# Performance work log

Measured on AMD Instinct MI355X. Metric: run time of the kernel, lower is better.

## Reference

```python
import math
import jax, jax.numpy as jnp
import numpy as np

B, S, HID = 1, 2048, 2048
H, D = 32, 64            # heads, head_dim = HID // H
THETA = 10000.0
EPS = 1e-6
LAYER_IDX = 12
LAM_INIT = 0.8 - 0.6 * math.exp(-0.3 * LAYER_IDX)  # lambda_init_fn(layer_idx)
SCALE = 1.0 / math.sqrt(D)


def _rope_cos_sin(seq_len, dim):
    inv_freq = 1.0 / (THETA ** (np.arange(0, dim, 2, dtype=np.float64) / dim))
    freqs = np.outer(np.arange(seq_len, dtype=np.float64), inv_freq)
    emb = np.concatenate([freqs, freqs], axis=-1)  # [S, D] (llama duplicates freqs)
    return jnp.asarray(np.cos(emb), jnp.float32), jnp.asarray(np.sin(emb), jnp.float32)


def _rotate_half(x):
    return jnp.concatenate([-x[..., D // 2:], x[..., : D // 2]], axis=-1)


def _apply_rope(x, cos, sin):
    # x: [B, H, S, D]; cos/sin: [S, D] broadcast over B, H
    return x * cos + _rotate_half(x) * sin


def setup_inputs() -> dict:
    key = jax.random.key(0)
    ks = jax.random.split(key, 10)
    return {
        "hidden_states": jax.random.normal(ks[0], (B, S, HID), jnp.float32),
        "Wq": jax.random.normal(ks[1], (2 * HID, HID), jnp.float32) * 0.02,
        "Wk": jax.random.normal(ks[2], (2 * HID, HID), jnp.float32) * 0.02,
        "Wv": jax.random.normal(ks[3], (HID, HID), jnp.float32) * 0.02,
        "Wo": jax.random.normal(ks[4], (HID, HID), jnp.float32) * 0.02,
        "lambda_q1": jax.random.normal(ks[5], (D,), jnp.float32) * 0.1,
        "lambda_k1": jax.random.normal(ks[6], (D,), jnp.float32) * 0.1,
        "lambda_q2": jax.random.normal(ks[7], (D,), jnp.float32) * 0.1,
        "lambda_k2": jax.random.normal(ks[8], (D,), jnp.float32) * 0.1,
        "subln_w": jnp.ones((D,), jnp.float32),
    }


def reference(hidden_states, Wq, Wk, Wv, Wo,
              lambda_q1, lambda_k1, lambda_q2, lambda_k2, subln_w):
    # Projections (nn.Linear, no bias): x @ W.T
    q = hidden_states @ Wq.T                       # [B, S, 2*HID]
    k = hidden_states @ Wk.T                       # [B, S, 2*HID]
    v = hidden_states @ Wv.T                       # [B, S, HID]

    def to_heads(t):  # [B, S, H*D] -> [B, H, S, D]
        return t.reshape(B, S, H, D).transpose(0, 2, 1, 3)

    q1, q2 = jnp.split(q, 2, axis=-1)
    k1, k2 = jnp.split(k, 2, axis=-1)
    q1, q2, k1, k2, v = map(to_heads, (q1, q2, k1, k2, v))

    cos, sin = _rope_cos_sin(S, D)
    q1, k1 = _apply_rope(q1, cos, sin), _apply_rope(k1, cos, sin)
    q2, k2 = _apply_rope(q2, cos, sin), _apply_rope(k2, cos, sin)

    # Causal additive mask [S, S]
    causal = jnp.tril(jnp.ones((S, S), bool))
    neg_inf = jnp.finfo(jnp.float32).min
    mask = jnp.where(causal, 0.0, neg_inf)

    s1 = jnp.einsum("bhqd,bhkd->bhqk", q1, k1) * SCALE + mask
    s2 = jnp.einsum("bhqd,bhkd->bhqk", q2, k2) * SCALE + mask

    lam = (jnp.exp(jnp.sum(lambda_q1 * lambda_k1))
           - jnp.exp(jnp.sum(lambda_q2 * lambda_k2)) + LAM_INIT)

    attn_w = jax.nn.softmax(s1, axis=-1) - lam * jax.nn.softmax(s2, axis=-1)
    attn = jnp.einsum("bhqk,bhkd->bhqd", attn_w, v)  # [B, H, S, D]

    # Head-wise RMSNorm (LlamaRMSNorm over value_head_dim)
    var = jnp.mean(jnp.square(attn), axis=-1, keepdims=True)
    attn = attn * jax.lax.rsqrt(var + EPS) * subln_w
    attn = attn * (1.0 - LAM_INIT)

    out = attn.transpose(0, 2, 1, 3).reshape(B, S, HID) @ Wo.T
    return out
```

## Files before the change

kernel.cpp:

```cpp
#include <hip/hip_runtime.h>


typedef __bf16 bf16;
typedef __bf16 bf16x4 __attribute__((ext_vector_type(4)));
typedef __bf16 bf16x8 __attribute__((ext_vector_type(8)));
typedef float  f32x4  __attribute__((ext_vector_type(4)));

#define MFMA(a, b, c) __builtin_amdgcn_mfma_f32_16x16x32_bf16((a), (b), (c), 0, 0, 0)

#define S_LEN   2048
#define HID_DIM 2048
#define NHEAD   32
#define HD      64
#define QKV_N   10240
#define LAM_INIT 0.7836057665316245f
#define ONE_MINUS_LAM_INIT 0.21639423346837553f
#define QSCALE  0.18033688011112042f
#define RMS_EPS 1e-6f

__device__ __forceinline__ void gld16(const void* g, void* l) {
    __builtin_amdgcn_global_load_lds(
        (const __attribute__((address_space(1))) void*)g,
        (__attribute__((address_space(3))) void*)l, 16, 0, 0);
}

__global__ void cvt_f32_bf16(const float* __restrict__ src, bf16* __restrict__ dst, int n) {
    int i = (blockIdx.x * 256 + threadIdx.x) * 4;
    if (i + 3 < n) {
        float4 v = *(const float4*)(src + i);
        bf16x4 o = { (bf16)v.x, (bf16)v.y, (bf16)v.z, (bf16)v.w };
        *(bf16x4*)(dst + i) = o;
    }
}

__global__ void lam_kernel(const float* __restrict__ lq1, const float* __restrict__ lk1,
                           const float* __restrict__ lq2, const float* __restrict__ lk2,
                           float* __restrict__ out) {
    int t = threadIdx.x;
    float a = lq1[t] * lk1[t];
    float b = lq2[t] * lk2[t];
    #pragma unroll
    for (int off = 32; off > 0; off >>= 1) {
        a += __shfl_xor(a, off, 64);
        b += __shfl_xor(b, off, 64);
    }
    if (t == 0) out[0] = expf(a) - expf(b) + LAM_INIT;
}

template<int OUT_BF16>
__global__ __launch_bounds__(256, 2)
void gemm_bt(const bf16* __restrict__ A, const bf16* __restrict__ B,
             void* __restrict__ Cout, int M, int N, int K) {
    __shared__ __align__(16) bf16 As[128 * 32];
    __shared__ __align__(16) bf16 Bs[128 * 32];
    const int tid  = threadIdx.x;
    const int wave = tid >> 6, lane = tid & 63;
    const int wm = wave >> 1, wn = wave & 1;
    const int l = lane & 15, quad = lane >> 4;
    const int m0 = blockIdx.y * 128, n0 = blockIdx.x * 128;

    f32x4 acc[4][4];
    #pragma unroll
    for (int i = 0; i < 4; ++i)
        #pragma unroll
        for (int j = 0; j < 4; ++j) acc[i][j] = (f32x4){0.f, 0.f, 0.f, 0.f};

    const int r0 = tid >> 2, c0 = (tid & 3) * 8;
    const bf16* Ag = A + (size_t)(m0 + r0) * K + c0;
    const bf16* Bg = B + (size_t)(n0 + r0) * K + c0;
    bf16* As0 = As + tid * 8;
    bf16* Bs0 = Bs + tid * 8;

    for (int kt = 0; kt < K; kt += 32) {
        __syncthreads();
        gld16(Ag + kt, As0);
        gld16(Ag + (size_t)64 * K + kt, As0 + 2048);
        gld16(Bg + kt, Bs0);
        gld16(Bg + (size_t)64 * K + kt, Bs0 + 2048);
        __syncthreads();

        bf16x8 af[4], bfr[4];
        #pragma unroll
        for (int mi = 0; mi < 4; ++mi)
            af[mi] = *(const bf16x8*)(As + (wm * 64 + mi * 16 + l) * 32 + quad * 8);
        #pragma unroll
        for (int ni = 0; ni < 4; ++ni)
            bfr[ni] = *(const bf16x8*)(Bs + (wn * 64 + ni * 16 + l) * 32 + quad * 8);
        #pragma unroll
        for (int mi = 0; mi < 4; ++mi)
            #pragma unroll
            for (int ni = 0; ni < 4; ++ni)
                acc[mi][ni] = MFMA(af[mi], bfr[ni], acc[mi][ni]);
    }

    #pragma unroll
    for (int mi = 0; mi < 4; ++mi)
        #pragma unroll
        for (int ni = 0; ni < 4; ++ni)
            #pragma unroll
            for (int r = 0; r < 4; ++r) {
                const int row = m0 + wm * 64 + mi * 16 + quad * 4 + r;
                const int col = n0 + wn * 64 + ni * 16 + l;
                const float v = acc[mi][ni][r];
                if (OUT_BF16) ((bf16*)Cout)[(size_t)row * N + col] = (bf16)v;
                else          ((float*)Cout)[(size_t)row * N + col] = v;
            }
}

__global__ __launch_bounds__(256)
void rope_split(const bf16* __restrict__ qkv,
                bf16* __restrict__ Q1, bf16* __restrict__ K1,
                bf16* __restrict__ Q2, bf16* __restrict__ K2,
                bf16* __restrict__ Vt) {
    const int h = blockIdx.y;
    const int s0 = blockIdx.x * 64;
    const int t = threadIdx.x;
    const int d = t & 63, sr = t >> 6;
    __shared__ __align__(16) bf16 vt_lds[64][72];

    const int i = d & 31;
    const float invf = exp2f(-(float)i * 0.4152410118609203f);
    const float sign = (d < 32) ? -1.0f : 1.0f;

    for (int it = 0; it < 16; ++it) {
        const int s = s0 + it * 4 + sr;
        const bf16* row = qkv + (size_t)s * QKV_N;
        const int cb  = h * 64 + d;
        const int cbo = h * 64 + (d ^ 32);
        const float ang = (float)s * invf;
        const float cs = cosf(ang), sn = sinf(ang);
        const float q1v = (float)row[cb],         q1o = (float)row[cbo];
        const float q2v = (float)row[2048 + cb],  q2o = (float)row[2048 + cbo];
        const float k1v = (float)row[4096 + cb],  k1o = (float)row[4096 + cbo];
        const float k2v = (float)row[6144 + cb],  k2o = (float)row[6144 + cbo];
        const float vv  = (float)row[8192 + cb];
        const size_t o = ((size_t)h * S_LEN + s) * HD + d;
        Q1[o] = (bf16)((q1v * cs + sign * q1o * sn) * QSCALE);
        Q2[o] = (bf16)((q2v * cs + sign * q2o * sn) * QSCALE);
        K1[o] = (bf16)(k1v * cs + sign * k1o * sn);
        K2[o] = (bf16)(k2v * cs + sign * k2o * sn);
        vt_lds[d][it * 4 + sr] = (bf16)vv;
    }
    __syncthreads();
    const int dd = t >> 2, cg = t & 3;
    bf16x8 w0 = *(const bf16x8*)(&vt_lds[dd][cg * 16]);
    bf16x8 w1 = *(const bf16x8*)(&vt_lds[dd][cg * 16 + 8]);
    bf16* dst = Vt + ((size_t)h * HD + dd) * S_LEN + s0 + cg * 16;
    *(bf16x8*)(dst)     = w0;
    *(bf16x8*)(dst + 8) = w1;
}

__global__ __launch_bounds__(256, 2)
void diff_attn(const bf16* __restrict__ Q1, const bf16* __restrict__ K1,
               const bf16* __restrict__ Q2, const bf16* __restrict__ K2,
               const bf16* __restrict__ Vt, const float* __restrict__ lam_p,
               const float* __restrict__ subln_w, bf16* __restrict__ attn_out) {
    const int bid  = blockIdx.x;
    const int h    = (bid >> 1) & 31;
    const int idx  = bid >> 6;
    const int qb   = (bid & 1) ? idx : (15 - idx);
    const int q0   = qb * 128;
    const int tid  = threadIdx.x;
    const int wave = tid >> 6, lane = tid & 63;
    const int sid  = wave >> 1, half = wave & 1;
    const int l    = lane & 15, quad = lane >> 4;
    const int q0w  = q0 + half * 64;

    __shared__ __align__(16) char smem[61440];
    bf16* K1s = (bf16*)smem;
    bf16* K2s = (bf16*)(smem + 8192);
    bf16* Vts = (bf16*)(smem + 16384);
    bf16* Pw  = (bf16*)(smem + 24576 + wave * 9216);

    const bf16* Qh  = (sid ? Q2 : Q1) + ((size_t)h * S_LEN + q0w) * HD;
    const bf16* K1g = K1 + (size_t)h * S_LEN * HD;
    const bf16* K2g = K2 + (size_t)h * S_LEN * HD;
    const bf16* Vtg = Vt + (size_t)h * HD * S_LEN;
    const bf16* Ksm = sid ? K2s : K1s;

    const int rr  = tid >> 3;
    const int csw = ((tid & 7) ^ (rr & 7)) * 8;
    bf16* l1 = K1s + tid * 8;
    bf16* l2 = K2s + tid * 8;
    bf16* lv = Vts + tid * 8;

    bf16x8 qf[4][2];
    #pragma unroll
    for (int ni = 0; ni < 4; ++ni)
        #pragma unroll
        for (int ks = 0; ks < 2; ++ks)
            qf[ni][ks] = *(const bf16x8*)(Qh + (ni * 16 + l) * HD + ks * 32 + quad * 8);

    f32x4 O[4][4];
    #pragma unroll
    for (int mi = 0; mi < 4; ++mi)
        #pragma unroll
        for (int ni = 0; ni < 4; ++ni)
            O[mi][ni] = (f32x4){0.f, 0.f, 0.f, 0.f};
    float csum[4] = {0.f, 0.f, 0.f, 0.f};

    const int T = 2 * qb + 2;
    const int sw8 = l & 7;
    for (int t = 0; t < T; ++t) {
        const int kv0 = t * 64;
        __syncthreads();
        {
            const bf16* k1p = K1g + (size_t)(kv0 + rr) * HD + csw;
            const bf16* k2p = K2g + (size_t)(kv0 + rr) * HD + csw;
            const bf16* vtp = Vtg + (size_t)rr * S_LEN + kv0 + csw;
            gld16(k1p, l1);
            gld16(k1p + (size_t)32 * HD, l1 + 2048);
            gld16(k2p, l2);
            gld16(k2p + (size_t)32 * HD, l2 + 2048);
            gld16(vtp, lv);
            gld16(vtp + (size_t)32 * S_LEN, lv + 2048);
        }
        __syncthreads();

        if (kv0 <= q0w) {
            const bool diag = (kv0 == q0w);

            #pragma unroll
            for (int mi = 0; mi < 4; ++mi) {
                const int krow = (mi * 16 + l) * 64;
                bf16x8 ka0 = *(const bf16x8*)(Ksm + krow + ((quad ^ sw8) << 3));
                bf16x8 ka1 = *(const bf16x8*)(Ksm + krow + (((4 + quad) ^ sw8) << 3));
                #pragma unroll
                for (int ni = 0; ni < 4; ++ni) {
                    f32x4 c = (f32x4){0.f, 0.f, 0.f, 0.f};
                    c = MFMA(ka0, qf[ni][0], c);
                    c = MFMA(ka1, qf[ni][1], c);
                    bf16x4 pk;
                    float lsum = 0.f;
                    #pragma unroll
                    for (int r = 0; r < 4; ++r) {
                        float p = __builtin_amdgcn_exp2f(c[r]);
                        if (diag && (mi * 16 + quad * 4 + r > ni * 16 + l)) p = 0.f;
                        lsum += p;
                        pk[r] = (bf16)p;
                    }
                    csum[ni] += lsum;
                    *(bf16x4*)(Pw + (ni * 16 + l) * 72 + mi * 16 + quad * 4) = pk;
                }
            }

            bf16x8 vb[2][4];
            #pragma unroll
            for (int ks = 0; ks < 2; ++ks)
                #pragma unroll
                for (int ni = 0; ni < 4; ++ni)
                    vb[ks][ni] = *(const bf16x8*)(Vts + (ni * 16 + l) * 64 +
                                                  ((((ks << 2) + quad) ^ sw8) << 3));

            asm volatile("s_waitcnt lgkmcnt(0)" ::: "memory");

            #pragma unroll
            for (int ks = 0; ks < 2; ++ks) {
                bf16x8 pa[4];
                #pragma unroll
                for (int mi = 0; mi < 4; ++mi)
                    pa[mi] = *(const bf16x8*)(Pw + (mi * 16 + l) * 72 + ks * 32 + quad * 8);
                #pragma unroll
                for (int ni = 0; ni < 4; ++ni)
                    #pragma unroll
                    for (int mi = 0; mi < 4; ++mi)
                        O[mi][ni] = MFMA(pa[mi], vb[ks][ni], O[mi][ni]);
            }
        }
    }

    __syncthreads();
    float* epi = (float*)(smem + half * 16640);

    #pragma unroll
    for (int ni = 0; ni < 4; ++ni) {
        csum[ni] += __shfl_xor(csum[ni], 16, 64);
        csum[ni] += __shfl_xor(csum[ni], 32, 64);
    }

    if (sid == 1) {
        const float lam = lam_p[0];
        #pragma unroll
        for (int mi = 0; mi < 4; ++mi)
            #pragma unroll
            for (int r = 0; r < 4; ++r) {
                const float inv = lam / __shfl(csum[mi], quad * 4 + r, 64);
                const int row = mi * 16 + quad * 4 + r;
                #pragma unroll
                for (int ni = 0; ni < 4; ++ni)
                    epi[row * 65 + ni * 16 + l] = O[mi][ni][r] * inv;
            }
    }
    __syncthreads();

    if (sid == 0) {
        float sw[4];
        #pragma unroll
        for (int ni = 0; ni < 4; ++ni) sw[ni] = subln_w[ni * 16 + l];

        #pragma unroll
        for (int mi = 0; mi < 4; ++mi) {
            float inv1[4];
            #pragma unroll
            for (int r = 0; r < 4; ++r)
                inv1[r] = 1.0f / __shfl(csum[mi], quad * 4 + r, 64);

            float v[4][4]; float ssq[4] = {0.f, 0.f, 0.f, 0.f};
            #pragma unroll
            for (int ni = 0; ni < 4; ++ni)
                #pragma unroll
                for (int r = 0; r < 4; ++r) {
                    const int row = mi * 16 + quad * 4 + r;
                    const float x = O[mi][ni][r] * inv1[r] - epi[row * 65 + ni * 16 + l];
                    v[ni][r] = x;
                    ssq[r] += x * x;
                }
            #pragma unroll
            for (int r = 0; r < 4; ++r) {
                float s = ssq[r];
                s += __shfl_xor(s, 1, 64);
                s += __shfl_xor(s, 2, 64);
                s += __shfl_xor(s, 4, 64);
                s += __shfl_xor(s, 8, 64);
                ssq[r] = rsqrtf(s * (1.0f / 64.0f) + RMS_EPS) * ONE_MINUS_LAM_INIT;
            }
            #pragma unroll
            for (int ni = 0; ni < 4; ++ni)
                #pragma unroll
                for (int r = 0; r < 4; ++r) {
                    const int row = q0w + mi * 16 + quad * 4 + r;
                    attn_out[(size_t)row * HID_DIM + h * 64 + ni * 16 + l] =
                        (bf16)(v[ni][r] * ssq[r] * sw[ni]);
                }
        }
    }
}

extern "C" void kernel_launch(void* const* d_in, const int* in_sizes, int n_in,
                              void* d_out, int out_size, void* d_ws, size_t ws_size,
                              hipStream_t stream) {
    const float* hs  = (const float*)d_in[0];
    const float* Wq  = (const float*)d_in[1];
    const float* Wk  = (const float*)d_in[2];
    const float* Wv  = (const float*)d_in[3];
    const float* Wo  = (const float*)d_in[4];
    const float* lq1 = (const float*)d_in[5];
    const float* lk1 = (const float*)d_in[6];
    const float* lq2 = (const float*)d_in[7];
    const float* lk2 = (const float*)d_in[8];
    const float* slw = (const float*)d_in[9];

    if (ws_size < 151000000u) return;

    char* ws = (char*)d_ws;
    bf16*  hsb  = (bf16*)(ws);
    bf16*  Wb   = (bf16*)(ws + 8388608);
    bf16*  Wob  = (bf16*)(ws + 50331648);
    bf16*  qkv  = (bf16*)(ws + 58720256);
    bf16*  Q1b  = (bf16*)(ws + 100663296);
    bf16*  K1b  = (bf16*)(ws + 109051904);
    bf16*  Q2b  = (bf16*)(ws + 117440512);
    bf16*  K2b  = (bf16*)(ws + 125829120);
    bf16*  Vtb  = (bf16*)(ws + 134217728);
    bf16*  abuf = (bf16*)(ws + 142606336);
    float* lamp = (float*)(ws + 150994944);

    cvt_f32_bf16<<<4096, 256, 0, stream>>>(hs, hsb, 4194304);
    cvt_f32_bf16<<<8192, 256, 0, stream>>>(Wq, Wb, 8388608);
    cvt_f32_bf16<<<8192, 256, 0, stream>>>(Wk, Wb + 8388608, 8388608);
    cvt_f32_bf16<<<4096, 256, 0, stream>>>(Wv, Wb + 16777216, 4194304);
    cvt_f32_bf16<<<4096, 256, 0, stream>>>(Wo, Wob, 4194304);
    lam_kernel<<<1, 64, 0, stream>>>(lq1, lk1, lq2, lk2, lamp);

    gemm_bt<1><<<dim3(QKV_N / 128, S_LEN / 128), 256, 0, stream>>>(
        hsb, Wb, qkv, S_LEN, QKV_N, HID_DIM);

    rope_split<<<dim3(S_LEN / 64, NHEAD), 256, 0, stream>>>(qkv, Q1b, K1b, Q2b, K2b, Vtb);

    diff_attn<<<512, 256, 0, stream>>>(Q1b, K1b, Q2b, K2b, Vtb, lamp, slw, abuf);

    gemm_bt<0><<<dim3(HID_DIM / 128, S_LEN / 128), 256, 0, stream>>>(
        abuf, Wob, d_out, S_LEN, HID_DIM, HID_DIM);
}
```

Baseline: 405.1 us.

## Merge conversion kernels, widen GEMM K-tile with swizzled LDS, split-K output projection

New measurement: 369.4 us. -8.8%, faster.

```diff
diff --git a/kernel.cpp b/kernel.cpp
--- a/kernel.cpp
+++ b/kernel.cpp
@@ -24,40 +24,52 @@
         (__attribute__((address_space(3))) void*)l, 16, 0, 0);
 }
 
-__global__ void cvt_f32_bf16(const float* __restrict__ src, bf16* __restrict__ dst, int n) {
-    int i = (blockIdx.x * 256 + threadIdx.x) * 4;
-    if (i + 3 < n) {
-        float4 v = *(const float4*)(src + i);
-        bf16x4 o = { (bf16)v.x, (bf16)v.y, (bf16)v.z, (bf16)v.w };
-        *(bf16x4*)(dst + i) = o;
-    }
-}
-
-__global__ void lam_kernel(const float* __restrict__ lq1, const float* __restrict__ lk1,
-                           const float* __restrict__ lq2, const float* __restrict__ lk2,
-                           float* __restrict__ out) {
-    int t = threadIdx.x;
-    float a = lq1[t] * lk1[t];
-    float b = lq2[t] * lk2[t];
-    #pragma unroll
-    for (int off = 32; off > 0; off >>= 1) {
-        a += __shfl_xor(a, off, 64);
-        b += __shfl_xor(b, off, 64);
-    }
-    if (t == 0) out[0] = expf(a) - expf(b) + LAM_INIT;
-}
-
-template<int OUT_BF16>
-__global__ __launch_bounds__(256, 2)
+__global__ void cvt_all(const float* __restrict__ hs, const float* __restrict__ Wq,
+                        const float* __restrict__ Wk, const float* __restrict__ Wv,
+                        const float* __restrict__ Wo,
+                        const float* __restrict__ lq1, const float* __restrict__ lk1,
+                        const float* __restrict__ lq2, const float* __restrict__ lk2,
+                        bf16* __restrict__ hsb, bf16* __restrict__ Wb,
+                        bf16* __restrict__ Wob, float* __restrict__ lam_out) {
+    const int bid = blockIdx.x;
+    if (bid >= 28672) {
+        const int t = threadIdx.x;
+        if (t < 64) {
+            float a = lq1[t] * lk1[t];
+            float b = lq2[t] * lk2[t];
+            #pragma unroll
+            for (int off = 32; off > 0; off >>= 1) {
+                a += __shfl_xor(a, off, 64);
+                b += __shfl_xor(b, off, 64);
+            }
+            if (t == 0) lam_out[0] = expf(a) - expf(b) + LAM_INIT;
+        }
+        return;
+    }
+    const float* src; bf16* dst; int off;
+    if      (bid <  4096) { src = hs; dst = hsb;            off = bid;         }
+    else if (bid < 12288) { src = Wq; dst = Wb;             off = bid - 4096;  }
+    else if (bid < 20480) { src = Wk; dst = Wb +  8388608;  off = bid - 12288; }
+    else if (bid < 24576) { src = Wv; dst = Wb + 16777216;  off = bid - 20480; }
+    else                  { src = Wo; dst = Wob;            off = bid - 24576; }
+    const int i = off * 1024 + threadIdx.x * 4;
+    float4 v = *(const float4*)(src + i);
+    bf16x4 o = { (bf16)v.x, (bf16)v.y, (bf16)v.z, (bf16)v.w };
+    *(bf16x4*)(dst + i) = o;
+}
+
+template<int OUT_MODE>
+__global__ __launch_bounds__(256, 3)
 void gemm_bt(const bf16* __restrict__ A, const bf16* __restrict__ B,
-             void* __restrict__ Cout, int M, int N, int K) {
-    __shared__ __align__(16) bf16 As[128 * 32];
-    __shared__ __align__(16) bf16 Bs[128 * 32];
+             void* __restrict__ Cout, int M, int N, int K_total, int K_part) {
+    __shared__ __align__(16) bf16 As[128 * 64];
+    __shared__ __align__(16) bf16 Bs[128 * 64];
     const int tid  = threadIdx.x;
     const int wave = tid >> 6, lane = tid & 63;
     const int wm = wave >> 1, wn = wave & 1;
     const int l = lane & 15, quad = lane >> 4;
     const int m0 = blockIdx.y * 128, n0 = blockIdx.x * 128;
+    const int kz = blockIdx.z * K_part;
 
     f32x4 acc[4][4];
     #pragma unroll
@@ -65,34 +77,40 @@
         #pragma unroll
         for (int j = 0; j < 4; ++j) acc[i][j] = (f32x4){0.f, 0.f, 0.f, 0.f};
 
-    const int r0 = tid >> 2, c0 = (tid & 3) * 8;
-    const bf16* Ag = A + (size_t)(m0 + r0) * K + c0;
-    const bf16* Bg = B + (size_t)(n0 + r0) * K + c0;
-    bf16* As0 = As + tid * 8;
-    bf16* Bs0 = Bs + tid * 8;
-
-    for (int kt = 0; kt < K; kt += 32) {
+    const int rr  = tid >> 3;
+    const int csw = ((tid & 7) ^ (rr & 7)) * 8;
+    const bf16* Ag = A + (size_t)(m0 + rr) * K_total + kz + csw;
+    const bf16* Bg = B + (size_t)(n0 + rr) * K_total + kz + csw;
+
+    for (int kt = 0; kt < K_part; kt += 64) {
         __syncthreads();
-        gld16(Ag + kt, As0);
-        gld16(Ag + (size_t)64 * K + kt, As0 + 2048);
-        gld16(Bg + kt, Bs0);
-        gld16(Bg + (size_t)64 * K + kt, Bs0 + 2048);
+        #pragma unroll
+        for (int j = 0; j < 4; ++j) {
+            gld16(Ag + (size_t)(32 * j) * K_total + kt, As + j * 2048 + tid * 8);
+            gld16(Bg + (size_t)(32 * j) * K_total + kt, Bs + j * 2048 + tid * 8);
+        }
         __syncthreads();
 
-        bf16x8 af[4], bfr[4];
-        #pragma unroll
-        for (int mi = 0; mi < 4; ++mi)
-            af[mi] = *(const bf16x8*)(As + (wm * 64 + mi * 16 + l) * 32 + quad * 8);
-        #pragma unroll
-        for (int ni = 0; ni < 4; ++ni)
-            bfr[ni] = *(const bf16x8*)(Bs + (wn * 64 + ni * 16 + l) * 32 + quad * 8);
-        #pragma unroll
-        for (int mi = 0; mi < 4; ++mi)
+        #pragma unroll
+        for (int ks = 0; ks < 2; ++ks) {
+            const int co = (((ks << 2) | quad) ^ (l & 7)) << 3;
+            bf16x8 af[4], bfr[4];
+            #pragma unroll
+            for (int mi = 0; mi < 4; ++mi)
+                af[mi] = *(const bf16x8*)(As + (wm * 64 + mi * 16 + l) * 64 + co);
             #pragma unroll
             for (int ni = 0; ni < 4; ++ni)
-                acc[mi][ni] = MFMA(af[mi], bfr[ni], acc[mi][ni]);
-    }
-
+                bfr[ni] = *(const bf16x8*)(Bs + (wn * 64 + ni * 16 + l) * 64 + co);
+            #pragma unroll
+            for (int mi = 0; mi < 4; ++mi)
+                #pragma unroll
+                for (int ni = 0; ni < 4; ++ni)
+                    acc[mi][ni] = MFMA(af[mi], bfr[ni], acc[mi][ni]);
+        }
+    }
+
+    float* Pf = (OUT_MODE == 2)
+              ? ((float*)Cout + (size_t)blockIdx.z * M * N) : (float*)Cout;
     #pragma unroll
     for (int mi = 0; mi < 4; ++mi)
         #pragma unroll
@@ -102,9 +120,17 @@
                 const int row = m0 + wm * 64 + mi * 16 + quad * 4 + r;
                 const int col = n0 + wn * 64 + ni * 16 + l;
                 const float v = acc[mi][ni][r];
-                if (OUT_BF16) ((bf16*)Cout)[(size_t)row * N + col] = (bf16)v;
-                else          ((float*)Cout)[(size_t)row * N + col] = v;
-            }
+                if (OUT_MODE == 1) ((bf16*)Cout)[(size_t)row * N + col] = (bf16)v;
+                else               Pf[(size_t)row * N + col] = v;
+            }
+}
+
+__global__ void reduce_add(const float* __restrict__ p, float* __restrict__ out, int n) {
+    const int i = (blockIdx.x * 256 + threadIdx.x) * 4;
+    float4 a = *(const float4*)(p + i);
+    float4 b = *(const float4*)(p + n + i);
+    float4 o = { a.x + b.x, a.y + b.y, a.z + b.z, a.w + b.w };
+    *(float4*)(out + i) = o;
 }
 
 __global__ __launch_bounds__(256)
@@ -357,6 +383,7 @@
     bf16*  Wb   = (bf16*)(ws + 8388608);
     bf16*  Wob  = (bf16*)(ws + 50331648);
     bf16*  qkv  = (bf16*)(ws + 58720256);
+    float* part = (float*)(ws + 58720256);
     bf16*  Q1b  = (bf16*)(ws + 100663296);
     bf16*  K1b  = (bf16*)(ws + 109051904);
     bf16*  Q2b  = (bf16*)(ws + 117440512);
@@ -365,20 +392,17 @@
     bf16*  abuf = (bf16*)(ws + 142606336);
     float* lamp = (float*)(ws + 150994944);
 
-    cvt_f32_bf16<<<4096, 256, 0, stream>>>(hs, hsb, 4194304);
-    cvt_f32_bf16<<<8192, 256, 0, stream>>>(Wq, Wb, 8388608);
-    cvt_f32_bf16<<<8192, 256, 0, stream>>>(Wk, Wb + 8388608, 8388608);
-    cvt_f32_bf16<<<4096, 256, 0, stream>>>(Wv, Wb + 16777216, 4194304);
-    cvt_f32_bf16<<<4096, 256, 0, stream>>>(Wo, Wob, 4194304);
-    lam_kernel<<<1, 64, 0, stream>>>(lq1, lk1, lq2, lk2, lamp);
-
-    gemm_bt<1><<<dim3(QKV_N / 128, S_LEN / 128), 256, 0, stream>>>(
-        hsb, Wb, qkv, S_LEN, QKV_N, HID_DIM);
+    cvt_all<<<28673, 256, 0, stream>>>(hs, Wq, Wk, Wv, Wo, lq1, lk1, lq2, lk2,
+                                       hsb, Wb, Wob, lamp);
+
+    gemm_bt<1><<<dim3(QKV_N / 128, S_LEN / 128, 1), 256, 0, stream>>>(
+        hsb, Wb, qkv, S_LEN, QKV_N, HID_DIM, HID_DIM);
 
     rope_split<<<dim3(S_LEN / 64, NHEAD), 256, 0, stream>>>(qkv, Q1b, K1b, Q2b, K2b, Vtb);
 
     diff_attn<<<512, 256, 0, stream>>>(Q1b, K1b, Q2b, K2b, Vtb, lamp, slw, abuf);
 
-    gemm_bt<0><<<dim3(HID_DIM / 128, S_LEN / 128), 256, 0, stream>>>(
-        abuf, Wob, d_out, S_LEN, HID_DIM, HID_DIM);
-}
+    gemm_bt<2><<<dim3(HID_DIM / 128, S_LEN / 128, 2), 256, 0, stream>>>(
+        abuf, Wob, part, S_LEN, HID_DIM, HID_DIM, HID_DIM / 2);
+    reduce_add<<<4096, 256, 0, stream>>>(part, (float*)d_out, S_LEN * HID_DIM);
+}
```
